# Kernel tuning notes

Hardware: AMD Instinct MI355X
Metric: run time of the kernel (lower is better)

Reference implementation:

```python
import jax, jax.numpy as jnp
import numpy as np

HIDDEN = 2048
NUM_HEADS = 16
HEAD_DIM = HIDDEN // NUM_HEADS
BATCH, SEQ = 2, 2048


def setup_inputs() -> dict:
    key = jax.random.key(0)
    ks = jax.random.split(key, 9)
    s = 1.0 / np.sqrt(HIDDEN)
    return {
        "hidden_state": jax.random.normal(ks[0], (BATCH, SEQ, HIDDEN), dtype=jnp.float32),
        "Wq": jax.random.normal(ks[1], (HIDDEN, HIDDEN), dtype=jnp.float32) * s,
        "bq": jax.random.normal(ks[2], (HIDDEN,), dtype=jnp.float32) * 0.01,
        "Wk": jax.random.normal(ks[3], (HIDDEN, HIDDEN), dtype=jnp.float32) * s,
        "bk": jax.random.normal(ks[4], (HIDDEN,), dtype=jnp.float32) * 0.01,
        "Wv": jax.random.normal(ks[5], (HIDDEN, HIDDEN), dtype=jnp.float32) * s,
        "bv": jax.random.normal(ks[6], (HIDDEN,), dtype=jnp.float32) * 0.01,
        "Wo": jax.random.normal(ks[7], (HIDDEN, HIDDEN), dtype=jnp.float32) * s,
        "bo": jax.random.normal(ks[8], (HIDDEN,), dtype=jnp.float32) * 0.01,
    }


def _split_heads(x):
    # (B, S, H*D) -> (B, H, S, D)
    b, s, _ = x.shape
    return x.reshape(b, s, NUM_HEADS, HEAD_DIM).transpose(0, 2, 1, 3)


def reference(hidden_state, Wq, bq, Wk, bk, Wv, bv, Wo, bo):
    q = _split_heads(hidden_state @ Wq + bq)
    k = _split_heads(hidden_state @ Wk + bk)
    v = _split_heads(hidden_state @ Wv + bv)
    scale = 1.0 / jnp.sqrt(jnp.asarray(HEAD_DIM, dtype=hidden_state.dtype))
    scores = jnp.einsum("bhqd,bhkd->bhqk", q, k) * scale  # (B,H,S,S)
    probs = jax.nn.softmax(scores, axis=-1)
    out = jnp.einsum("bhqk,bhkd->bhqd", probs, v)  # (B,H,S,D)
    b, h, s, d = out.shape
    out = out.transpose(0, 2, 1, 3).reshape(b, s, h * d)  # merge heads
    return out @ Wo + bo
```

## Files before the change

kernel.cpp:

```cpp
#include <hip/hip_runtime.h>
#include <math.h>

typedef __bf16 bf16;
typedef __bf16 bf16x4 __attribute__((ext_vector_type(4)));
typedef __bf16 bf16x8 __attribute__((ext_vector_type(8)));
typedef float  f32x4  __attribute__((ext_vector_type(4)));

#define HIDDEN 2048
#define NH     16
#define HD     128
#define BATCH  2
#define SEQ    2048
#define MROWS  (BATCH*SEQ)
#define NQKV   (3*HIDDEN)

__device__ __forceinline__ void async16(const bf16* g, bf16* l) {
  __builtin_amdgcn_global_load_lds(
      (const __attribute__((address_space(1))) void*)g,
      (__attribute__((address_space(3))) void*)l, 16, 0, 0);
}

__global__ __launch_bounds__(256) void cast_f32_bf16_kernel(
    const float* __restrict__ src, bf16* __restrict__ dst, int n4) {
  int i = blockIdx.x * 256 + threadIdx.x;
  if (i >= n4) return;
  float4 f = ((const float4*)src)[i];
  bf16x4 o;
  o[0] = (bf16)f.x; o[1] = (bf16)f.y; o[2] = (bf16)f.z; o[3] = (bf16)f.w;
  ((bf16x4*)dst)[i] = o;
}

__global__ __launch_bounds__(256) void transpose_cast4_kernel(
    const float* __restrict__ s0, const float* __restrict__ s1,
    const float* __restrict__ s2, const float* __restrict__ s3,
    bf16* __restrict__ d0, bf16* __restrict__ d1,
    bf16* __restrict__ d2, bf16* __restrict__ d3) {
  const float* src; bf16* dst;
  switch (blockIdx.z) {
    case 0: src = s0; dst = d0; break;
    case 1: src = s1; dst = d1; break;
    case 2: src = s2; dst = d2; break;
    default: src = s3; dst = d3; break;
  }
  __shared__ float t[32][33];
  int x  = blockIdx.x * 32 + threadIdx.x;
  int y0 = blockIdx.y * 32;
#pragma unroll
  for (int i = 0; i < 32; i += 8)
    t[threadIdx.y + i][threadIdx.x] = src[(size_t)(y0 + threadIdx.y + i) * HIDDEN + x];
  __syncthreads();
  int xo  = blockIdx.y * 32 + threadIdx.x;
  int yo0 = blockIdx.x * 32;
#pragma unroll
  for (int i = 0; i < 32; i += 8)
    dst[(size_t)(yo0 + threadIdx.y + i) * HIDDEN + xo] = (bf16)t[threadIdx.x][threadIdx.y + i];
}

__global__ __launch_bounds__(256) void concat3_kernel(
    const float* __restrict__ a, const float* __restrict__ b,
    const float* __restrict__ c, float* __restrict__ dst) {
  int i = blockIdx.x * 256 + threadIdx.x;
  float v = (i < 2048) ? a[i] : (i < 4096 ? b[i - 2048] : c[i - 4096]);
  dst[i] = v;
}

__global__ __launch_bounds__(256) void transpose_v_kernel(
    const bf16* __restrict__ QKV, bf16* __restrict__ Vt) {
  __shared__ bf16 t[32][33];
  int bh = blockIdx.z, b = bh >> 4, h = bh & 15;
  const bf16* src = QKV + (size_t)b * SEQ * NQKV + 2 * HIDDEN + h * HD;
  bf16* dst = Vt + (size_t)bh * HD * SEQ;
  int s0 = blockIdx.x * 32, d0 = blockIdx.y * 32;
#pragma unroll
  for (int i = 0; i < 32; i += 8)
    t[threadIdx.y + i][threadIdx.x] = src[(size_t)(s0 + threadIdx.y + i) * NQKV + d0 + threadIdx.x];
  __syncthreads();
#pragma unroll
  for (int i = 0; i < 32; i += 8)
    dst[(size_t)(d0 + threadIdx.y + i) * SEQ + s0 + threadIdx.x] = t[threadIdx.x][threadIdx.y + i];
}

template <typename OutT>
__global__ __launch_bounds__(256) void gemm_bt_bias(
    const bf16* __restrict__ A, const bf16* __restrict__ Bt,
    const float* __restrict__ bias, OutT* __restrict__ C, int N, int K) {
  __shared__ bf16 Ash[128 * 64];
  __shared__ bf16 Bsh[128 * 64];
  const int tid = threadIdx.x;
  const int wave = tid >> 6, lane = tid & 63, quad = lane >> 4, l16 = lane & 15;
  const int wm = (wave & 1) * 64, wn = (wave >> 1) * 64;
  const int m0 = blockIdx.x * 128, n0 = blockIdx.y * 128;

  const f32x4 zero4 = {0.f, 0.f, 0.f, 0.f};
  f32x4 acc[4][4];
#pragma unroll
  for (int i = 0; i < 4; i++)
#pragma unroll
    for (int j = 0; j < 4; j++) acc[i][j] = zero4;

  const int crow = tid >> 3, ccc = tid & 7;
  const int cd = (ccc - crow) & 7;
  const int l7 = l16 & 7;

  const bf16* pa[4];
  const bf16* pb[4];
#pragma unroll
  for (int s = 0; s < 4; s++) {
    pa[s] = &A[(size_t)(m0 + s * 32 + crow) * K + cd * 8];
    pb[s] = &Bt[(size_t)(n0 + s * 32 + crow) * K + cd * 8];
  }

  for (int kt = 0; kt < K; kt += 64) {
    __syncthreads();
#pragma unroll
    for (int s = 0; s < 4; s++) {
      async16(pa[s], &Ash[s * 2048 + tid * 8]);
      async16(pb[s], &Bsh[s * 2048 + tid * 8]);
      pa[s] += 64; pb[s] += 64;
    }
    __syncthreads();

#pragma unroll
    for (int kk = 0; kk < 2; kk++) {
      const int pc = (kk * 4 + quad + l7) & 7;
      bf16x8 af[4], bfr[4];
#pragma unroll
      for (int i = 0; i < 4; i++) af[i]  = *(const bf16x8*)&Ash[(wm + i * 16 + l16) * 64 + pc * 8];
#pragma unroll
      for (int j = 0; j < 4; j++) bfr[j] = *(const bf16x8*)&Bsh[(wn + j * 16 + l16) * 64 + pc * 8];
#pragma unroll
      for (int i = 0; i < 4; i++)
#pragma unroll
        for (int j = 0; j < 4; j++)
          acc[i][j] = __builtin_amdgcn_mfma_f32_16x16x32_bf16(af[i], bfr[j], acc[i][j], 0, 0, 0);
    }
  }

#pragma unroll
  for (int i = 0; i < 4; i++)
#pragma unroll
    for (int j = 0; j < 4; j++) {
      int n = n0 + wn + j * 16 + l16;
      float bv = bias[n];
#pragma unroll
      for (int r = 0; r < 4; r++) {
        int m = m0 + wm + i * 16 + quad * 4 + r;
        C[(size_t)m * N + n] = (OutT)(acc[i][j][r] + bv);
      }
    }
}

template <typename OutT>
__global__ __launch_bounds__(512, 2) void gemm_bt_bias_256(
    const bf16* __restrict__ A, const bf16* __restrict__ Bt,
    const float* __restrict__ bias, OutT* __restrict__ C, int N, int K) {
  __shared__ bf16 Ash[2][2][128 * 64];
  __shared__ bf16 Bsh[2][2][128 * 64];

  const int tid = threadIdx.x;
  const int wave = tid >> 6, lane = tid & 63, quad = lane >> 4, l16 = lane & 15, l7 = l16 & 7;
  const int hA = wave >> 2;
  const int wnq = wave & 3;
  const int hB = wnq >> 1, rB0 = (wnq & 1) * 64;
  const int m0 = blockIdx.x * 256, n0 = blockIdx.y * 256;

  const f32x4 zero4 = {0.f, 0.f, 0.f, 0.f};
  f32x4 acc[8][4];
#pragma unroll
  for (int i = 0; i < 8; i++)
#pragma unroll
    for (int j = 0; j < 4; j++) acc[i][j] = zero4;

  const int crow = tid >> 3, ccc = tid & 7;
  const int cd = (ccc - crow) & 7;

  const bf16* gA[2][2];
  const bf16* gB[2][2];
#pragma unroll
  for (int h = 0; h < 2; h++)
#pragma unroll
    for (int s = 0; s < 2; s++) {
      gA[h][s] = &A[(size_t)(m0 + h * 128 + s * 64 + crow) * K + cd * 8];
      gB[h][s] = &Bt[(size_t)(n0 + h * 128 + s * 64 + crow) * K + cd * 8];
    }

  auto stageA = [&](int buf, int h) {
    async16(gA[h][0], &Ash[buf][h][0 * 4096 + tid * 8]); gA[h][0] += 64;
    async16(gA[h][1], &Ash[buf][h][1 * 4096 + tid * 8]); gA[h][1] += 64;
  };
  auto stageB = [&](int buf, int h) {
    async16(gB[h][0], &Bsh[buf][h][0 * 4096 + tid * 8]); gB[h][0] += 64;
    async16(gB[h][1], &Bsh[buf][h][1 * 4096 + tid * 8]); gB[h][1] += 64;
  };

  const int NT = K >> 6;

  stageA(0, 0); stageA(0, 1); stageB(0, 0); stageB(0, 1);
  stageA(1, 0);
  asm volatile("s_waitcnt vmcnt(2)" ::: "memory");
  __builtin_amdgcn_s_barrier();

  for (int t = 0; t < NT; ++t) {
    const int cur = t & 1, nxt = cur ^ 1;
    const bool s1 = (t + 1 < NT), s2 = (t + 2 < NT);
    const bf16* Ab = Ash[cur][hA];
    const bf16* Bb = Bsh[cur][hB];

    bf16x8 af[4][2], bfr[4][2];

#pragma unroll
    for (int mi = 0; mi < 4; mi++)
#pragma unroll
      for (int ks = 0; ks < 2; ks++)
        af[mi][ks] = *(const bf16x8*)&Ab[(mi * 16 + l16) * 64 + (((ks * 4 + quad) + l7) & 7) * 8];
#pragma unroll
    for (int ni = 0; ni < 2; ni++)
#pragma unroll
      for (int ks = 0; ks < 2; ks++)
        bfr[ni][ks] = *(const bf16x8*)&Bb[(rB0 + ni * 16 + l16) * 64 + (((ks * 4 + quad) + l7) & 7) * 8];
    if (s1) stageA(nxt, 1);
    __builtin_amdgcn_s_barrier();
    asm volatile("s_waitcnt lgkmcnt(0)" ::: "memory");
    __builtin_amdgcn_sched_barrier(0);
    __builtin_amdgcn_s_setprio(1);
#pragma unroll
    for (int ks = 0; ks < 2; ks++)
#pragma unroll
      for (int mi = 0; mi < 4; mi++)
#pragma unroll
        for (int ni = 0; ni < 2; ni++)
          acc[mi][ni] = __builtin_amdgcn_mfma_f32_16x16x32_bf16(af[mi][ks], bfr[ni][ks], acc[mi][ni], 0, 0, 0);
    __builtin_amdgcn_s_setprio(0);
    __builtin_amdgcn_s_barrier();

#pragma unroll
    for (int ni = 2; ni < 4; ni++)
#pragma unroll
      for (int ks = 0; ks < 2; ks++)
        bfr[ni][ks] = *(const bf16x8*)&Bb[(rB0 + ni * 16 + l16) * 64 + (((ks * 4 + quad) + l7) & 7) * 8];
    if (s1) stageB(nxt, 0);
    __builtin_amdgcn_s_barrier();
    asm volatile("s_waitcnt lgkmcnt(0)" ::: "memory");
    __builtin_amdgcn_sched_barrier(0);
    __builtin_amdgcn_s_setprio(1);
#pragma unroll
    for (int ks = 0; ks < 2; ks++)
#pragma unroll
      for (int mi = 0; mi < 4; mi++)
#pragma unroll
        for (int ni = 2; ni < 4; ni++)
          acc[mi][ni] = __builtin_amdgcn_mfma_f32_16x16x32_bf16(af[mi][ks], bfr[ni][ks], acc[mi][ni], 0, 0, 0);
    __builtin_amdgcn_s_setprio(0);
    __builtin_amdgcn_s_barrier();

#pragma unroll
    for (int mi = 0; mi < 4; mi++)
#pragma unroll
      for (int ks = 0; ks < 2; ks++)
        af[mi][ks] = *(const bf16x8*)&Ab[((mi + 4) * 16 + l16) * 64 + (((ks * 4 + quad) + l7) & 7) * 8];
    if (s1) stageB(nxt, 1);
    __builtin_amdgcn_s_barrier();
    asm volatile("s_waitcnt lgkmcnt(0)" ::: "memory");
    __builtin_amdgcn_sched_barrier(0);
    __builtin_amdgcn_s_setprio(1);
#pragma unroll
    for (int ks = 0; ks < 2; ks++)
#pragma unroll
      for (int mi = 0; mi < 4; mi++)
#pragma unroll
        for (int ni = 0; ni < 2; ni++)
          acc[4 + mi][ni] = __builtin_amdgcn_mfma_f32_16x16x32_bf16(af[mi][ks], bfr[ni][ks], acc[4 + mi][ni], 0, 0, 0);
    __builtin_amdgcn_s_setprio(0);
    __builtin_amdgcn_s_barrier();

    if (s2) stageA(cur, 0);
    __builtin_amdgcn_s_setprio(1);
#pragma unroll
    for (int ks = 0; ks < 2; ks++)
#pragma unroll
      for (int mi = 0; mi < 4; mi++)
#pragma unroll
        for (int ni = 2; ni < 4; ni++)
          acc[4 + mi][ni] = __builtin_amdgcn_mfma_f32_16x16x32_bf16(af[mi][ks], bfr[ni][ks], acc[4 + mi][ni], 0, 0, 0);
    __builtin_amdgcn_s_setprio(0);
    if (s2) asm volatile("s_waitcnt vmcnt(2)" ::: "memory");
    else    asm volatile("s_waitcnt vmcnt(0)" ::: "memory");
    __builtin_amdgcn_s_barrier();
  }

#pragma unroll
  for (int mi = 0; mi < 8; mi++)
#pragma unroll
    for (int ni = 0; ni < 4; ni++) {
      int n = n0 + wnq * 64 + ni * 16 + l16;
      float bv = bias[n];
#pragma unroll
      for (int r = 0; r < 4; r++) {
        int m = m0 + hA * 128 + mi * 16 + quad * 4 + r;
        C[(size_t)m * N + n] = (OutT)(acc[mi][ni][r] + bv);
      }
    }
}

#define KTS   64
#define PPAD  72

__global__ __launch_bounds__(256, 2) void flash_attn_kernel(
    const bf16* __restrict__ QKV, const bf16* __restrict__ Vt, bf16* __restrict__ O) {
  const int bh = blockIdx.y, b = bh >> 4, h = bh & 15;
  const int q0 = blockIdx.x * 128;
  const int tid = threadIdx.x, wave = tid >> 6, lane = tid & 63, quad = lane >> 4, l16 = lane & 15;

  const bf16* Qb  = QKV + (size_t)b * SEQ * NQKV + h * HD;
  const bf16* Kb  = QKV + (size_t)b * SEQ * NQKV + HIDDEN + h * HD;
  const bf16* Vtb = Vt + (size_t)bh * HD * SEQ;

  __shared__ bf16 Ksh[KTS * HD];
  __shared__ bf16 Vsh[HD * KTS];
  __shared__ bf16 Psh[128 * PPAD];

  const int qrow = q0 + wave * 32;
  const float sc = 0.08838834764831845f * 1.44269504088896340f;

  bf16x8 qf[2][4];
#pragma unroll
  for (int mt = 0; mt < 2; mt++)
#pragma unroll
    for (int kk = 0; kk < 4; kk++) {
      bf16x8 t = *(const bf16x8*)&Qb[(size_t)(qrow + mt * 16 + l16) * NQKV + kk * 32 + quad * 8];
#pragma unroll
      for (int j = 0; j < 8; j++) t[j] = (bf16)((float)t[j] * sc);
      qf[mt][kk] = t;
    }

  const f32x4 zero4 = {0.f, 0.f, 0.f, 0.f};
  f32x4 oacc[2][8];
#pragma unroll
  for (int mt = 0; mt < 2; mt++)
#pragma unroll
    for (int nt = 0; nt < 8; nt++) oacc[mt][nt] = zero4;

  float lrun[2] = {0.f, 0.f};

  const int krp = tid >> 4, kpp = tid & 15;
  const int vrp = tid >> 3, vpp = tid & 7;
  const int l7 = l16 & 7;

  const bf16* pk[4];
  const bf16* pv[4];
#pragma unroll
  for (int s = 0; s < 4; s++) {
    int r  = s * 16 + krp;
    pk[s] = &Kb[(size_t)r * NQKV + (kpp ^ (r & 7)) * 8];
    int rv = s * 32 + vrp;
    pv[s] = &Vtb[(size_t)rv * SEQ + (vpp ^ (rv & 7)) * 8];
  }

  for (int kt = 0; kt < SEQ; kt += KTS) {
    __syncthreads();
#pragma unroll
    for (int s = 0; s < 4; s++) {
      async16(pk[s], &Ksh[s * 2048 + tid * 8]);
      async16(pv[s], &Vsh[s * 2048 + tid * 8]);
      pk[s] += (size_t)KTS * NQKV;
      pv[s] += KTS;
    }
    __syncthreads();

    f32x4 st[2][4];
#pragma unroll
    for (int mt = 0; mt < 2; mt++)
#pragma unroll
      for (int nt = 0; nt < 4; nt++) st[mt][nt] = zero4;
#pragma unroll
    for (int kk = 0; kk < 4; kk++) {
      const int p = (4 * kk + quad) ^ l7;
      bf16x8 kf[4];
#pragma unroll
      for (int nt = 0; nt < 4; nt++)
        kf[nt] = *(const bf16x8*)&Ksh[(nt * 16 + l16) * HD + p * 8];
#pragma unroll
      for (int mt = 0; mt < 2; mt++)
#pragma unroll
        for (int nt = 0; nt < 4; nt++)
          st[mt][nt] = __builtin_amdgcn_mfma_f32_16x16x32_bf16(kf[nt], qf[mt][kk], st[mt][nt], 0, 0, 0);
    }

    float rs[2] = {0.f, 0.f};
#pragma unroll
    for (int mt = 0; mt < 2; mt++)
#pragma unroll
      for (int nt = 0; nt < 4; nt++) {
        bf16x4 pk4;
#pragma unroll
        for (int r = 0; r < 4; r++) {
          float p = exp2f(st[mt][nt][r]);
          rs[mt] += p;
          pk4[r] = (bf16)p;
        }
        *(bf16x4*)&Psh[(wave * 32 + mt * 16 + l16) * PPAD + nt * 16 + quad * 4] = pk4;
      }
#pragma unroll
    for (int mt = 0; mt < 2; mt++) {
      float t = rs[mt];
      t += __shfl_xor(t, 16);
      t += __shfl_xor(t, 32);
      lrun[mt] += t;
    }

#pragma unroll
    for (int kk2 = 0; kk2 < 2; kk2++) {
      bf16x8 pf[2], vf[8];
#pragma unroll
      for (int mt = 0; mt < 2; mt++)
        pf[mt] = *(const bf16x8*)&Psh[(wave * 32 + mt * 16 + l16) * PPAD + kk2 * 32 + quad * 8];
#pragma unroll
      for (int nt = 0; nt < 8; nt++) {
        int p = (4 * kk2 + quad) ^ l7;
        vf[nt] = *(const bf16x8*)&Vsh[(nt * 16 + l16) * KTS + p * 8];
      }
#pragma unroll
      for (int mt = 0; mt < 2; mt++)
#pragma unroll
        for (int nt = 0; nt < 8; nt++)
          oacc[mt][nt] = __builtin_amdgcn_mfma_f32_16x16x32_bf16(pf[mt], vf[nt], oacc[mt][nt], 0, 0, 0);
    }
  }

#pragma unroll
  for (int mt = 0; mt < 2; mt++) {
    float inv[4];
#pragma unroll
    for (int r = 0; r < 4; r++)
      inv[r] = 1.0f / __shfl(lrun[mt], (lane & 48) | (quad * 4 + r));
#pragma unroll
    for (int nt = 0; nt < 8; nt++)
#pragma unroll
      for (int r = 0; r < 4; r++) {
        int q = qrow + mt * 16 + quad * 4 + r;
        int d = nt * 16 + l16;
        O[(size_t)(b * SEQ + q) * HIDDEN + h * HD + d] = (bf16)(oacc[mt][nt][r] * inv[r]);
      }
  }
}

extern "C" void kernel_launch(void* const* d_in, const int* in_sizes, int n_in,
                              void* d_out, int out_size, void* d_ws, size_t ws_size,
                              hipStream_t stream) {
  const float* hs = (const float*)d_in[0];
  const float* Wq = (const float*)d_in[1];
  const float* bq = (const float*)d_in[2];
  const float* Wk = (const float*)d_in[3];
  const float* bk = (const float*)d_in[4];
  const float* Wv = (const float*)d_in[5];
  const float* bv = (const float*)d_in[6];
  const float* Wo = (const float*)d_in[7];
  const float* bo = (const float*)d_in[8];
  float* out = (float*)d_out;

  char* ws = (char*)d_ws;
  bf16*  Abf   = (bf16*)(ws);
  bf16*  WtQKV = (bf16*)(ws + 16777216);
  bf16*  WtO   = (bf16*)(ws + 41943040);
  float* biasQ = (float*)(ws + 50331648);
  bf16*  QKV   = (bf16*)(ws + 50356224);
  bf16*  VT    = (bf16*)(ws + 100687872);
  bf16*  Obf   = (bf16*)(ws + 117465088);

  dim3 tb(32, 8);
  cast_f32_bf16_kernel<<<8192, 256, 0, stream>>>(hs, Abf, 2097152);
  transpose_cast4_kernel<<<dim3(64, 64, 4), tb, 0, stream>>>(
      Wq, Wk, Wv, Wo,
      WtQKV, WtQKV + 2048 * 2048, WtQKV + 2 * 2048 * 2048, WtO);
  concat3_kernel<<<24, 256, 0, stream>>>(bq, bk, bv, biasQ);

  gemm_bt_bias_256<bf16><<<dim3(16, 24), 512, 0, stream>>>(Abf, WtQKV, biasQ, QKV, NQKV, HIDDEN);
  transpose_v_kernel<<<dim3(64, 4, 32), tb, 0, stream>>>(QKV, VT);
  flash_attn_kernel<<<dim3(16, 32), 256, 0, stream>>>(QKV, VT, Obf);
  gemm_bt_bias<float><<<dim3(32, 16), 256, 0, stream>>>(Obf, WtO, bo, out, HIDDEN, HIDDEN);
}
```

Measured before the change: 409.8 us.

## Double-buffer flash-attention K/V tiles and deepen GEMM prefetch pipeline

The flash attention kernel now double-buffers K and V tiles in LDS, prefetching the next tile while the current one is computed, instead of syncing around a single buffer. It also XOR-swizzles the P buffer in place of padding, remaps block indices to group heads for better L2 locality, and raises MFMA priority. The GEMM prologue now stages two full A/B stages up front and issues whole-stage prefetches two iterations ahead. The cost is more LDS per block, which may reduce occupancy with launch bounds of 2 blocks.

```diff
diff --git a/kernel.cpp b/kernel.cpp
--- a/kernel.cpp
+++ b/kernel.cpp
@@ -195,14 +195,14 @@
 
   const int NT = K >> 6;
 
-  stageA(0, 0); stageA(0, 1); stageB(0, 0); stageB(0, 1);
-  stageA(1, 0);
-  asm volatile("s_waitcnt vmcnt(2)" ::: "memory");
+  stageB(0, 0); stageB(0, 1); stageA(0, 0); stageA(0, 1);
+  stageB(1, 0); stageB(1, 1); stageA(1, 0); stageA(1, 1);
+  asm volatile("s_waitcnt vmcnt(8)" ::: "memory");
   __builtin_amdgcn_s_barrier();
 
   for (int t = 0; t < NT; ++t) {
-    const int cur = t & 1, nxt = cur ^ 1;
-    const bool s1 = (t + 1 < NT), s2 = (t + 2 < NT);
+    const int cur = t & 1;
+    const bool st = (t + 2 < NT);
     const bf16* Ab = Ash[cur][hA];
     const bf16* Bb = Bsh[cur][hB];
 
@@ -218,7 +218,6 @@
 #pragma unroll
       for (int ks = 0; ks < 2; ks++)
         bfr[ni][ks] = *(const bf16x8*)&Bb[(rB0 + ni * 16 + l16) * 64 + (((ks * 4 + quad) + l7) & 7) * 8];
-    if (s1) stageA(nxt, 1);
     __builtin_amdgcn_s_barrier();
     asm volatile("s_waitcnt lgkmcnt(0)" ::: "memory");
     __builtin_amdgcn_sched_barrier(0);
@@ -238,7 +237,6 @@
 #pragma unroll
       for (int ks = 0; ks < 2; ks++)
         bfr[ni][ks] = *(const bf16x8*)&Bb[(rB0 + ni * 16 + l16) * 64 + (((ks * 4 + quad) + l7) & 7) * 8];
-    if (s1) stageB(nxt, 0);
     __builtin_amdgcn_s_barrier();
     asm volatile("s_waitcnt lgkmcnt(0)" ::: "memory");
     __builtin_amdgcn_sched_barrier(0);
@@ -258,7 +256,7 @@
 #pragma unroll
       for (int ks = 0; ks < 2; ks++)
         af[mi][ks] = *(const bf16x8*)&Ab[((mi + 4) * 16 + l16) * 64 + (((ks * 4 + quad) + l7) & 7) * 8];
-    if (s1) stageB(nxt, 1);
+    if (st) { stageB(cur, 0); stageB(cur, 1); }
     __builtin_amdgcn_s_barrier();
     asm volatile("s_waitcnt lgkmcnt(0)" ::: "memory");
     __builtin_amdgcn_sched_barrier(0);
@@ -273,7 +271,7 @@
     __builtin_amdgcn_s_setprio(0);
     __builtin_amdgcn_s_barrier();
 
-    if (s2) stageA(cur, 0);
+    if (st) { stageA(cur, 0); stageA(cur, 1); }
     __builtin_amdgcn_s_setprio(1);
 #pragma unroll
     for (int ks = 0; ks < 2; ks++)
@@ -283,7 +281,7 @@
         for (int ni = 2; ni < 4; ni++)
           acc[4 + mi][ni] = __builtin_amdgcn_mfma_f32_16x16x32_bf16(af[mi][ks], bfr[ni][ks], acc[4 + mi][ni], 0, 0, 0);
     __builtin_amdgcn_s_setprio(0);
-    if (s2) asm volatile("s_waitcnt vmcnt(2)" ::: "memory");
+    if (st) asm volatile("s_waitcnt vmcnt(8)" ::: "memory");
     else    asm volatile("s_waitcnt vmcnt(0)" ::: "memory");
     __builtin_amdgcn_s_barrier();
   }
@@ -303,21 +301,22 @@
 }
 
 #define KTS   64
-#define PPAD  72
 
 __global__ __launch_bounds__(256, 2) void flash_attn_kernel(
     const bf16* __restrict__ QKV, const bf16* __restrict__ Vt, bf16* __restrict__ O) {
-  const int bh = blockIdx.y, b = bh >> 4, h = bh & 15;
-  const int q0 = blockIdx.x * 128;
+  const int fid = blockIdx.x + 16 * blockIdx.y;
+  const int nid = (fid & 7) * 64 + (fid >> 3);
+  const int bh = nid >> 4, b = bh >> 4, h = bh & 15;
+  const int q0 = (nid & 15) * 128;
   const int tid = threadIdx.x, wave = tid >> 6, lane = tid & 63, quad = lane >> 4, l16 = lane & 15;
 
   const bf16* Qb  = QKV + (size_t)b * SEQ * NQKV + h * HD;
   const bf16* Kb  = QKV + (size_t)b * SEQ * NQKV + HIDDEN + h * HD;
   const bf16* Vtb = Vt + (size_t)bh * HD * SEQ;
 
-  __shared__ bf16 Ksh[KTS * HD];
-  __shared__ bf16 Vsh[HD * KTS];
-  __shared__ bf16 Psh[128 * PPAD];
+  __shared__ bf16 Ksh[2][KTS * HD];
+  __shared__ bf16 Vsh[2][HD * KTS];
+  __shared__ bf16 Psh[128 * 64];
 
   const int qrow = q0 + wave * 32;
   const float sc = 0.08838834764831845f * 1.44269504088896340f;
@@ -356,16 +355,30 @@
     pv[s] = &Vtb[(size_t)rv * SEQ + (vpp ^ (rv & 7)) * 8];
   }
 
-  for (int kt = 0; kt < SEQ; kt += KTS) {
-    __syncthreads();
-#pragma unroll
-    for (int s = 0; s < 4; s++) {
-      async16(pk[s], &Ksh[s * 2048 + tid * 8]);
-      async16(pv[s], &Vsh[s * 2048 + tid * 8]);
-      pk[s] += (size_t)KTS * NQKV;
-      pv[s] += KTS;
-    }
-    __syncthreads();
+#pragma unroll
+  for (int s = 0; s < 4; s++) {
+    async16(pk[s], &Ksh[0][s * 2048 + tid * 8]);
+    async16(pv[s], &Vsh[0][s * 2048 + tid * 8]);
+    pk[s] += (size_t)KTS * NQKV;
+    pv[s] += KTS;
+  }
+
+  const int NT = SEQ / KTS;
+  for (int t = 0; t < NT; ++t) {
+    const int cur = t & 1;
+    if (t + 1 < NT) {
+#pragma unroll
+      for (int s = 0; s < 4; s++) {
+        async16(pk[s], &Ksh[cur ^ 1][s * 2048 + tid * 8]);
+        async16(pv[s], &Vsh[cur ^ 1][s * 2048 + tid * 8]);
+        pk[s] += (size_t)KTS * NQKV;
+        pv[s] += KTS;
+      }
+      asm volatile("s_waitcnt vmcnt(8)" ::: "memory");
+    } else {
+      asm volatile("s_waitcnt vmcnt(0)" ::: "memory");
+    }
+    __builtin_amdgcn_s_barrier();
 
     f32x4 st[2][4];
 #pragma unroll
@@ -378,12 +391,14 @@
       bf16x8 kf[4];
 #pragma unroll
       for (int nt = 0; nt < 4; nt++)
-        kf[nt] = *(const bf16x8*)&Ksh[(nt * 16 + l16) * HD + p * 8];
+        kf[nt] = *(const bf16x8*)&Ksh[cur][(nt * 16 + l16) * HD + p * 8];
+      __builtin_amdgcn_s_setprio(1);
 #pragma unroll
       for (int mt = 0; mt < 2; mt++)
 #pragma unroll
         for (int nt = 0; nt < 4; nt++)
           st[mt][nt] = __builtin_amdgcn_mfma_f32_16x16x32_bf16(kf[nt], qf[mt][kk], st[mt][nt], 0, 0, 0);
+      __builtin_amdgcn_s_setprio(0);
     }
 
     float rs[2] = {0.f, 0.f};
@@ -398,33 +413,42 @@
           rs[mt] += p;
           pk4[r] = (bf16)p;
         }
-        *(bf16x4*)&Psh[(wave * 32 + mt * 16 + l16) * PPAD + nt * 16 + quad * 4] = pk4;
+        int pbyte = ((wave * 32 + mt * 16 + l16) * 64 + nt * 16 + quad * 4) * 2;
+        pbyte ^= (l16 & 7) << 4;
+        *(bf16x4*)((char*)Psh + pbyte) = pk4;
       }
 #pragma unroll
     for (int mt = 0; mt < 2; mt++) {
-      float t = rs[mt];
-      t += __shfl_xor(t, 16);
-      t += __shfl_xor(t, 32);
-      lrun[mt] += t;
+      float t2 = rs[mt];
+      t2 += __shfl_xor(t2, 16);
+      t2 += __shfl_xor(t2, 32);
+      lrun[mt] += t2;
     }
 
 #pragma unroll
     for (int kk2 = 0; kk2 < 2; kk2++) {
       bf16x8 pf[2], vf[8];
 #pragma unroll
-      for (int mt = 0; mt < 2; mt++)
-        pf[mt] = *(const bf16x8*)&Psh[(wave * 32 + mt * 16 + l16) * PPAD + kk2 * 32 + quad * 8];
+      for (int mt = 0; mt < 2; mt++) {
+        int pbyte = ((wave * 32 + mt * 16 + l16) * 64 + kk2 * 32 + quad * 8) * 2;
+        pbyte ^= (l16 & 7) << 4;
+        pf[mt] = *(const bf16x8*)((char*)Psh + pbyte);
+      }
 #pragma unroll
       for (int nt = 0; nt < 8; nt++) {
         int p = (4 * kk2 + quad) ^ l7;
-        vf[nt] = *(const bf16x8*)&Vsh[(nt * 16 + l16) * KTS + p * 8];
-      }
+        vf[nt] = *(const bf16x8*)&Vsh[cur][(nt * 16 + l16) * KTS + p * 8];
+      }
+      __builtin_amdgcn_s_setprio(1);
 #pragma unroll
       for (int mt = 0; mt < 2; mt++)
 #pragma unroll
         for (int nt = 0; nt < 8; nt++)
           oacc[mt][nt] = __builtin_amdgcn_mfma_f32_16x16x32_bf16(pf[mt], vf[nt], oacc[mt][nt], 0, 0, 0);
-    }
+      __builtin_amdgcn_s_setprio(0);
+    }
+
+    __builtin_amdgcn_s_barrier();
   }
 
 #pragma unroll
```

Result: no change. 408.4 us (-0.3%).
